# Kernel optimization log

Hardware: AMD Instinct MI355X
Metric: run time of the kernel (lower is better)

## Reference

```python
import jax, jax.numpy as jnp
import numpy as np

B, N, DIN, DOUT, EIN, EOUT = 8, 256, 64, 64, 64, 64


def setup_inputs() -> dict:
    key = jax.random.key(0)
    ks = jax.random.split(key, 9)
    A = jax.random.randint(ks[0], (B, N, N), 0, 2).astype(jnp.float32)  # {0,1} connectivity
    emb_node = jax.random.normal(ks[1], (B, N, DIN), dtype=jnp.float32)
    emb_edge = jax.random.normal(ks[2], (B, N, N, EIN), dtype=jnp.float32)
    s_n = 1.0 / np.sqrt(DIN)
    s_e = 1.0 / np.sqrt(EIN)
    Wn = jax.random.uniform(ks[3], (DIN, DOUT), minval=-s_n, maxval=s_n)
    bn = jax.random.uniform(ks[4], (DOUT,), minval=-s_n, maxval=s_n)
    Wsn = jax.random.uniform(ks[5], (DIN, DOUT), minval=-s_n, maxval=s_n)
    bsn = jax.random.uniform(ks[6], (DOUT,), minval=-s_n, maxval=s_n)
    We = jax.random.uniform(ks[7], (EIN, EOUT), minval=-s_e, maxval=s_e)
    be = jax.random.uniform(ks[8], (EOUT,), minval=-s_e, maxval=s_e)
    return {"A": A, "emb_node": emb_node, "emb_edge": emb_edge,
            "Wn": Wn, "bn": bn, "Wsn": Wsn, "bsn": bsn, "We": We, "be": be}


def reference(A, emb_node, emb_edge, Wn, bn, Wsn, bsn, We, be):
    # mode=1 (default) of ChannelIndependentConv
    node_x = emb_node @ Wn + bn          # [B,N,DOUT]
    node_sx = emb_node @ Wsn + bsn       # [B,N,DOUT]
    edge_x = emb_edge @ We + be          # [B,N,N,EOUT]
    # mask edges by connectivity, then channel-independent aggregation:
    # out[b,i,c] = sum_j A[b,i,j] * edge_x[b,i,j,c] * node_x[b,j,c]
    Ae = A[..., None] * edge_x           # [B,N,N,EOUT]
    agg = jnp.einsum('bijc,bjc->bic', Ae, node_x)  # [B,N,DOUT]
    node_out = jax.nn.relu(agg) + jax.nn.relu(node_sx)
    edge_out = jax.nn.relu(edge_x)
    return node_out, edge_out
```

## Files before the change

### kernel.cpp

```cpp
#include <hip/hip_runtime.h>
#include <hip/hip_bf16.h>

#define BN   2048
#define NN   256
#define CH   64
#define RPC  32
#define NCHK 8
#define LDST 88

typedef __attribute__((ext_vector_type(8))) short short8;
typedef __attribute__((ext_vector_type(4))) short short4v;
typedef __attribute__((ext_vector_type(4))) float fv4;

static __device__ inline short f2bf(float f) {
  unsigned u = __float_as_uint(f);
  u += 0x7FFF + ((u >> 16) & 1);
  return (short)(u >> 16);
}
static __device__ inline short4v cvt4(fv4 v) {
  short4v r;
  r[0] = f2bf(v[0]); r[1] = f2bf(v[1]); r[2] = f2bf(v[2]); r[3] = f2bf(v[3]);
  return r;
}

__global__ __launch_bounds__(256) void node_kernel(
    const float* __restrict__ emb_node, const float* __restrict__ Wn,
    const float* __restrict__ bn, const float* __restrict__ Wsn,
    const float* __restrict__ bsn, float* __restrict__ node_x,
    float* __restrict__ rsx) {
  __shared__ float s_emb[4][CH];
  __shared__ float s_Wn[CH * CH];
  __shared__ float s_Ws[CH * CH];
  const int tid = threadIdx.x;
  const int r = tid >> 6;
  const int c = tid & 63;
  const int row = blockIdx.x * 4 + r;
#pragma unroll
  for (int i = 0; i < 4; ++i) {
    *(fv4*)&s_Wn[(i * 256 + tid) * 4] = *(const fv4*)&Wn[(i * 256 + tid) * 4];
    *(fv4*)&s_Ws[(i * 256 + tid) * 4] = *(const fv4*)&Wsn[(i * 256 + tid) * 4];
  }
  s_emb[r][c] = emb_node[row * CH + c];
  __syncthreads();
  float a1 = bn[c], a2 = bsn[c];
#pragma unroll
  for (int k = 0; k < CH; ++k) {
    const float e = s_emb[r][k];
    a1 = fmaf(e, s_Wn[k * CH + c], a1);
    a2 = fmaf(e, s_Ws[k * CH + c], a2);
  }
  node_x[row * CH + c] = a1;
  rsx[row * CH + c] = fmaxf(a2, 0.0f);
}

__global__ __launch_bounds__(256) void edge_mfma_kernel(
    const float* __restrict__ A, const float* __restrict__ emb_edge,
    const float* __restrict__ We, const float* __restrict__ be,
    const float* __restrict__ node_x, const float* __restrict__ rsx,
    float* __restrict__ node_out, float* __restrict__ edge_out) {
  const int bi   = blockIdx.x;
  const int b    = bi >> 8;
  const int tid  = threadIdx.x;
  const int lane = tid & 63;
  const int wave = tid >> 6;
  const int l15  = lane & 15;
  const int quad = lane >> 4;
  const int c    = wave * 16 + l15;

  __shared__ __align__(16) short sbuf[2][RPC * LDST];
  __shared__ float s_A[NN];

  short8 bfrag[2];
#pragma unroll
  for (int h = 0; h < 2; ++h)
#pragma unroll
    for (int j = 0; j < 8; ++j)
      bfrag[h][j] = f2bf(We[(h * 32 + quad * 8 + j) * CH + c]);
  const float bias = be[c];

  const float* __restrict__ ee = emb_edge + (size_t)bi * NN * CH;
  float*       __restrict__ eo = edge_out + (size_t)bi * NN * CH;
  const float* __restrict__ nx = node_x + (size_t)b * NN * CH;

  s_A[tid] = A[(size_t)bi * NN + tid];

  const int srow = tid >> 4;
  const int kcol = (tid & 15) * 4;

  fv4 st0 = *(const fv4*)(ee + tid * 4);
  fv4 st1 = *(const fv4*)(ee + 1024 + tid * 4);
  *(short4v*)&sbuf[0][srow * LDST + kcol] = cvt4(st0);
  *(short4v*)&sbuf[0][(16 + srow) * LDST + kcol] = cvt4(st1);

  float agg = 0.0f;

#pragma unroll 2
  for (int ch = 0; ch < NCHK; ++ch) {
    const int pb = ch & 1;
    if (ch + 1 < NCHK) {
      const float* cb = ee + (ch + 1) * (RPC * CH);
      st0 = *(const fv4*)(cb + tid * 4);
      st1 = *(const fv4*)(cb + 1024 + tid * 4);
    }
    __syncthreads();

#pragma unroll
    for (int half = 0; half < 2; ++half) {
      const int j0l = half * 16;
      const int j0  = ch * RPC + j0l;
      const fv4 av = *(const fv4*)&s_A[j0 + quad * 4];
      float nxv[4];
#pragma unroll
      for (int r = 0; r < 4; ++r)
        nxv[r] = nx[(j0 + quad * 4 + r) * CH + c];
      const short8 af0 =
          *(const short8*)&sbuf[pb][(j0l + l15) * LDST + quad * 8];
      const short8 af1 =
          *(const short8*)&sbuf[pb][(j0l + l15) * LDST + 32 + quad * 8];
      fv4 acc = {0.0f, 0.0f, 0.0f, 0.0f};
      acc = __builtin_amdgcn_mfma_f32_16x16x32_bf16(af0, bfrag[0], acc, 0, 0, 0);
      acc = __builtin_amdgcn_mfma_f32_16x16x32_bf16(af1, bfrag[1], acc, 0, 0, 0);
#pragma unroll
      for (int r = 0; r < 4; ++r) {
        const int row = j0 + quad * 4 + r;
        const float ex = acc[r] + bias;
        eo[row * CH + c] = fmaxf(ex, 0.0f);
        agg = fmaf(av[r] * ex, nxv[r], agg);
      }
    }

    if (ch + 1 < NCHK) {
      *(short4v*)&sbuf[pb ^ 1][srow * LDST + kcol] = cvt4(st0);
      *(short4v*)&sbuf[pb ^ 1][(16 + srow) * LDST + kcol] = cvt4(st1);
    }
  }

  agg += __shfl_xor(agg, 16, 64);
  agg += __shfl_xor(agg, 32, 64);
  if (quad == 0) {
    node_out[(size_t)bi * CH + c] =
        fmaxf(agg, 0.0f) + rsx[(size_t)bi * CH + c];
  }
}

extern "C" void kernel_launch(void* const* d_in, const int* in_sizes, int n_in,
                              void* d_out, int out_size, void* d_ws, size_t ws_size,
                              hipStream_t stream) {
  const float* A        = (const float*)d_in[0];
  const float* emb_node = (const float*)d_in[1];
  const float* emb_edge = (const float*)d_in[2];
  const float* Wn       = (const float*)d_in[3];
  const float* bn       = (const float*)d_in[4];
  const float* Wsn      = (const float*)d_in[5];
  const float* bsn      = (const float*)d_in[6];
  const float* We       = (const float*)d_in[7];
  const float* be       = (const float*)d_in[8];

  float* node_out = (float*)d_out;
  float* edge_out = (float*)d_out + (size_t)BN * CH;

  float* node_x = (float*)d_ws;
  float* rsx    = (float*)d_ws + (size_t)BN * CH;

  hipLaunchKernelGGL(node_kernel, dim3(BN / 4), dim3(256), 0, stream,
                     emb_node, Wn, bn, Wsn, bsn, node_x, rsx);
  hipLaunchKernelGGL(edge_mfma_kernel, dim3(BN), dim3(256), 0, stream,
                     A, emb_edge, We, be, node_x, rsx, node_out, edge_out);
}
```

Measured before the change: 259.4 us.

## Load edge rows directly into MFMA fragments, split rows across waves

Each wave now owns 64 rows of j and computes all 64 output channels, loading emb_edge straight from global memory into registers in MFMA A-fragment order. This removes the LDS staging buffer and the per-chunk barriers. Loads and stores use nontemporal hints, and per-wave partial aggregates are combined through LDS atomics before the final write. In exchange it uses more registers for four B-fragment sets and accumulators, and the global loads are 16-byte strided per lane rather than fully coalesced rows.

```diff
diff --git a/kernel.cpp b/kernel.cpp
--- a/kernel.cpp
+++ b/kernel.cpp
@@ -4,12 +4,8 @@
 #define BN   2048
 #define NN   256
 #define CH   64
-#define RPC  32
-#define NCHK 8
-#define LDST 88
 
 typedef __attribute__((ext_vector_type(8))) short short8;
-typedef __attribute__((ext_vector_type(4))) short short4v;
 typedef __attribute__((ext_vector_type(4))) float fv4;
 
 static __device__ inline short f2bf(float f) {
@@ -17,10 +13,11 @@
   u += 0x7FFF + ((u >> 16) & 1);
   return (short)(u >> 16);
 }
-static __device__ inline short4v cvt4(fv4 v) {
-  short4v r;
-  r[0] = f2bf(v[0]); r[1] = f2bf(v[1]); r[2] = f2bf(v[2]); r[3] = f2bf(v[3]);
-  return r;
+static __device__ inline short8 cvt8(fv4 a, fv4 b) {
+  short8 f;
+  f[0] = f2bf(a[0]); f[1] = f2bf(a[1]); f[2] = f2bf(a[2]); f[3] = f2bf(a[3]);
+  f[4] = f2bf(b[0]); f[5] = f2bf(b[1]); f[6] = f2bf(b[2]); f[7] = f2bf(b[3]);
+  return f;
 }
 
 __global__ __launch_bounds__(256) void node_kernel(
@@ -65,81 +62,98 @@
   const int wave = tid >> 6;
   const int l15  = lane & 15;
   const int quad = lane >> 4;
-  const int c    = wave * 16 + l15;
 
-  __shared__ __align__(16) short sbuf[2][RPC * LDST];
   __shared__ float s_A[NN];
+  __shared__ float s_agg[CH];
 
-  short8 bfrag[2];
+  s_A[tid] = A[(size_t)bi * NN + tid];
+  if (tid < CH) s_agg[tid] = 0.0f;
+
+  short8 bfrag[4][2];
+  float bias[4];
 #pragma unroll
-  for (int h = 0; h < 2; ++h)
+  for (int ct = 0; ct < 4; ++ct) {
+    const int c = 16 * ct + l15;
 #pragma unroll
-    for (int j = 0; j < 8; ++j)
-      bfrag[h][j] = f2bf(We[(h * 32 + quad * 8 + j) * CH + c]);
-  const float bias = be[c];
+    for (int h = 0; h < 2; ++h)
+#pragma unroll
+      for (int j = 0; j < 8; ++j)
+        bfrag[ct][h][j] = f2bf(We[(h * 32 + quad * 8 + j) * CH + c]);
+    bias[ct] = be[c];
+  }
 
   const float* __restrict__ ee = emb_edge + (size_t)bi * NN * CH;
   float*       __restrict__ eo = edge_out + (size_t)bi * NN * CH;
   const float* __restrict__ nx = node_x + (size_t)b * NN * CH;
 
-  s_A[tid] = A[(size_t)bi * NN + tid];
+  const int jbase = wave * 64;
+  __syncthreads();
 
-  const int srow = tid >> 4;
-  const int kcol = (tid & 15) * 4;
+  fv4 ld[2][4];
+#pragma unroll
+  for (int q = 0; q < 4; ++q) {
+    const float* p = ee + (size_t)(jbase + l15) * CH + quad * 8 + (q & 1) * 4 + (q >> 1) * 32;
+    ld[0][q] = __builtin_nontemporal_load((const fv4*)p);
+  }
 
-  fv4 st0 = *(const fv4*)(ee + tid * 4);
-  fv4 st1 = *(const fv4*)(ee + 1024 + tid * 4);
-  *(short4v*)&sbuf[0][srow * LDST + kcol] = cvt4(st0);
-  *(short4v*)&sbuf[0][(16 + srow) * LDST + kcol] = cvt4(st1);
-
-  float agg = 0.0f;
-
-#pragma unroll 2
-  for (int ch = 0; ch < NCHK; ++ch) {
-    const int pb = ch & 1;
-    if (ch + 1 < NCHK) {
-      const float* cb = ee + (ch + 1) * (RPC * CH);
-      st0 = *(const fv4*)(cb + tid * 4);
-      st1 = *(const fv4*)(cb + 1024 + tid * 4);
-    }
-    __syncthreads();
+  float agg[4] = {0.0f, 0.0f, 0.0f, 0.0f};
 
 #pragma unroll
-    for (int half = 0; half < 2; ++half) {
-      const int j0l = half * 16;
-      const int j0  = ch * RPC + j0l;
-      const fv4 av = *(const fv4*)&s_A[j0 + quad * 4];
-      float nxv[4];
+  for (int t = 0; t < 4; ++t) {
+    const int pb = t & 1;
+    if (t < 3) {
+#pragma unroll
+      for (int q = 0; q < 4; ++q) {
+        const float* p = ee + (size_t)(jbase + (t + 1) * 16 + l15) * CH +
+                         quad * 8 + (q & 1) * 4 + (q >> 1) * 32;
+        ld[pb ^ 1][q] = __builtin_nontemporal_load((const fv4*)p);
+      }
+    }
+    const int rbase = jbase + t * 16 + quad * 4;
+    float nxv[4][4];
+#pragma unroll
+    for (int ct = 0; ct < 4; ++ct)
 #pragma unroll
       for (int r = 0; r < 4; ++r)
-        nxv[r] = nx[(j0 + quad * 4 + r) * CH + c];
-      const short8 af0 =
-          *(const short8*)&sbuf[pb][(j0l + l15) * LDST + quad * 8];
-      const short8 af1 =
-          *(const short8*)&sbuf[pb][(j0l + l15) * LDST + 32 + quad * 8];
-      fv4 acc = {0.0f, 0.0f, 0.0f, 0.0f};
-      acc = __builtin_amdgcn_mfma_f32_16x16x32_bf16(af0, bfrag[0], acc, 0, 0, 0);
-      acc = __builtin_amdgcn_mfma_f32_16x16x32_bf16(af1, bfrag[1], acc, 0, 0, 0);
+        nxv[ct][r] = nx[(rbase + r) * CH + 16 * ct + l15];
+
+    const short8 af0 = cvt8(ld[pb][0], ld[pb][1]);
+    const short8 af1 = cvt8(ld[pb][2], ld[pb][3]);
+    fv4 acc[4];
+#pragma unroll
+    for (int ct = 0; ct < 4; ++ct) {
+      acc[ct] = fv4{0.0f, 0.0f, 0.0f, 0.0f};
+      acc[ct] = __builtin_amdgcn_mfma_f32_16x16x32_bf16(af0, bfrag[ct][0], acc[ct], 0, 0, 0);
+      acc[ct] = __builtin_amdgcn_mfma_f32_16x16x32_bf16(af1, bfrag[ct][1], acc[ct], 0, 0, 0);
+    }
+
+    const fv4 av = *(const fv4*)&s_A[rbase];
+#pragma unroll
+    for (int ct = 0; ct < 4; ++ct) {
+      const int c = 16 * ct + l15;
 #pragma unroll
       for (int r = 0; r < 4; ++r) {
-        const int row = j0 + quad * 4 + r;
-        const float ex = acc[r] + bias;
-        eo[row * CH + c] = fmaxf(ex, 0.0f);
-        agg = fmaf(av[r] * ex, nxv[r], agg);
+        const float ex = acc[ct][r] + bias[ct];
+        __builtin_nontemporal_store(fmaxf(ex, 0.0f), eo + (rbase + r) * CH + c);
+        agg[ct] = fmaf(av[r] * ex, nxv[ct][r], agg[ct]);
       }
-    }
-
-    if (ch + 1 < NCHK) {
-      *(short4v*)&sbuf[pb ^ 1][srow * LDST + kcol] = cvt4(st0);
-      *(short4v*)&sbuf[pb ^ 1][(16 + srow) * LDST + kcol] = cvt4(st1);
     }
   }
 
-  agg += __shfl_xor(agg, 16, 64);
-  agg += __shfl_xor(agg, 32, 64);
+#pragma unroll
+  for (int ct = 0; ct < 4; ++ct) {
+    agg[ct] += __shfl_xor(agg[ct], 16, 64);
+    agg[ct] += __shfl_xor(agg[ct], 32, 64);
+  }
   if (quad == 0) {
-    node_out[(size_t)bi * CH + c] =
-        fmaxf(agg, 0.0f) + rsx[(size_t)bi * CH + c];
+#pragma unroll
+    for (int ct = 0; ct < 4; ++ct)
+      atomicAdd(&s_agg[16 * ct + l15], agg[ct]);
+  }
+  __syncthreads();
+  if (tid < CH) {
+    node_out[(size_t)bi * CH + tid] =
+        fmaxf(s_agg[tid], 0.0f) + rsx[(size_t)bi * CH + tid];
   }
 }
 
```

New measurement: 269.0 us. 1.04x slower.
